# Kernel tuning notes

Measured on AMD Instinct MI355X. Metric: run time of the kernel, lower is better.

Reference implementation:

```python
import jax, jax.numpy as jnp
import numpy as np

TEMPERATURE = 0.0005

def conv1d(x, w, b):
    # x: [B,Cin,T], w: [Cout,Cin,K], 'same' padding as ConvNorm (pad=(K-1)//2)
    pad = (w.shape[-1] - 1) // 2
    y = jax.lax.conv_general_dilated(x, w, window_strides=(1,), padding=[(pad, pad)],
                                     dimension_numbers=('NCH', 'OIH', 'NCH'))
    return y + b[None, :, None]

def setup_inputs() -> dict:
    key = jax.random.key(0)
    ks = jax.random.split(key, 20)
    B, C_MEL, C_TXT, C_ATT, T1, T2 = 32, 80, 512, 80, 1600, 400
    s = 0.02
    return {
        'queries': jax.random.normal(ks[0], (B, C_MEL, T1), jnp.float32),
        'keys': jax.random.normal(ks[1], (B, C_TXT, T2), jnp.float32),
        'mask': jax.random.randint(ks[2], (B, T2, 1), 0, 2).astype(bool),
        'attn_prior': jax.random.uniform(ks[3], (B, T1, T2), jnp.float32),
        'speaker_embed': jax.random.normal(ks[4], (B, C_TXT), jnp.float32),
        # key_proj: Conv(512->1024,k3) -> ReLU -> Conv(1024->80,k1)
        'Wk1': jax.random.normal(ks[5], (C_TXT * 2, C_TXT, 3)) * s,
        'bk1': jax.random.normal(ks[6], (C_TXT * 2,)) * s,
        'Wk2': jax.random.normal(ks[7], (C_ATT, C_TXT * 2, 1)) * s,
        'bk2': jax.random.normal(ks[8], (C_ATT,)) * s,
        # query_proj: Conv(80->160,k3) -> ReLU -> Conv(160->80,k1) -> ReLU -> Conv(80->80,k1)
        'Wq1': jax.random.normal(ks[9], (C_MEL * 2, C_MEL, 3)) * s,
        'bq1': jax.random.normal(ks[10], (C_MEL * 2,)) * s,
        'Wq2': jax.random.normal(ks[11], (C_MEL, C_MEL * 2, 1)) * s,
        'bq2': jax.random.normal(ks[12], (C_MEL,)) * s,
        'Wq3': jax.random.normal(ks[13], (C_ATT, C_MEL, 1)) * s,
        'bq3': jax.random.normal(ks[14], (C_ATT,)) * s,
        # speaker projections (multi_speaker=True)
        'Wks': jax.random.normal(ks[15], (C_TXT, C_TXT)) * s,
        'bks': jax.random.normal(ks[16], (C_TXT,)) * s,
        'Wqs': jax.random.normal(ks[17], (C_MEL, C_TXT)) * s,
        'bqs': jax.random.normal(ks[18], (C_MEL,)) * s,
    }

def reference(queries, keys, mask, attn_prior, speaker_embed,
              Wk1, bk1, Wk2, bk2, Wq1, bq1, Wq2, bq2, Wq3, bq3,
              Wks, bks, Wqs, bqs):
    # speaker conditioning: Linear(spk) broadcast over time, added channelwise
    keys = keys + (speaker_embed @ Wks.T + bks)[:, :, None]
    queries = queries + (speaker_embed @ Wqs.T + bqs)[:, :, None]
    # projections
    k = jax.nn.relu(conv1d(keys, Wk1, bk1))
    k = conv1d(k, Wk2, bk2)                      # [B, C_att, T2]
    q = jax.nn.relu(conv1d(queries, Wq1, bq1))
    q = jax.nn.relu(conv1d(q, Wq2, bq2))
    q = conv1d(q, Wq3, bq3)                      # [B, C_att, T1]
    # -temp * sum_c (q-k)^2 == -temp * (||q||^2 + ||k||^2 - 2 q.k)
    q2 = jnp.sum(q * q, axis=1)                  # [B, T1]
    k2 = jnp.sum(k * k, axis=1)                  # [B, T2]
    qk = jnp.einsum('bct,bcs->bts', q, k)        # [B, T1, T2]
    attn = -TEMPERATURE * (q2[:, :, None] + k2[:, None, :] - 2.0 * qk)
    attn = attn[:, None]                         # [B, 1, T1, T2]
    attn = jax.nn.log_softmax(attn, axis=3) + jnp.log(attn_prior[:, None] + 1e-8)
    attn_logprob = attn
    m = jnp.transpose(mask, (0, 2, 1))[:, :, None, :]  # [B,1,1,T2]
    attn = jnp.where(m, -jnp.inf, attn)
    attn = jax.nn.softmax(attn, axis=3)
    return attn, attn_logprob
```

## Files before the change

kernel.cpp:

```cpp
#include <hip/hip_runtime.h>
#include <math.h>

#define TEMP 0.0005f
#define B_    32
#define CMEL  80
#define CTXT  512
#define T1_   1600
#define T2_   400

typedef short short8 __attribute__((ext_vector_type(8)));
typedef float f32x4 __attribute__((ext_vector_type(4)));

__device__ inline unsigned short f2bf(float f) {
    unsigned u = __float_as_uint(f);
    u += 0x7FFF + ((u >> 16) & 1);
    return (unsigned short)(u >> 16);
}
__device__ inline unsigned pack2(float a, float b) {
    return (unsigned)f2bf(a) | ((unsigned)f2bf(b) << 16);
}
__device__ inline float bf2f(unsigned short v) { return __uint_as_float(((unsigned)v) << 16); }

__global__ void prep_kernel(const float* __restrict__ se,
                            const float* __restrict__ Wks, const float* __restrict__ bks,
                            const float* __restrict__ Wqs, const float* __restrict__ bqs,
                            float* __restrict__ kb, float* __restrict__ qb,
                            const float* __restrict__ Wk1, const float* __restrict__ Wk2,
                            const float* __restrict__ Wq1, const float* __restrict__ Wq2,
                            const float* __restrict__ Wq3,
                            unsigned short* __restrict__ Ab1, unsigned short* __restrict__ A2,
                            unsigned short* __restrict__ A3, unsigned short* __restrict__ A4,
                            unsigned short* __restrict__ A5) {
    if (blockIdx.x < 74) {
        int tid = blockIdx.x * blockDim.x + threadIdx.x;
        const int nk = B_ * CTXT;
        if (tid < nk) {
            int b = tid / CTXT, c = tid % CTXT;
            const float4* s4 = reinterpret_cast<const float4*>(se + b * CTXT);
            const float4* w4 = reinterpret_cast<const float4*>(Wks + (size_t)c * CTXT);
            float acc = bks[c];
            #pragma unroll 4
            for (int j = 0; j < CTXT / 4; ++j) {
                float4 a = s4[j], w = w4[j];
                acc += a.x * w.x + a.y * w.y + a.z * w.z + a.w * w.w;
            }
            kb[tid] = acc;
        } else if (tid < nk + B_ * CMEL) {
            int t = tid - nk;
            int b = t / CMEL, c = t % CMEL;
            const float4* s4 = reinterpret_cast<const float4*>(se + b * CTXT);
            const float4* w4 = reinterpret_cast<const float4*>(Wqs + (size_t)c * CTXT);
            float acc = bqs[c];
            #pragma unroll 4
            for (int j = 0; j < CTXT / 4; ++j) {
                float4 a = s4[j], w = w4[j];
                acc += a.x * w.x + a.y * w.y + a.z * w.z + a.w * w.w;
            }
            qb[t] = acc;
        }
        return;
    }
    int e = (blockIdx.x - 74) * 256 + threadIdx.x;
    const int n1 = 1572864, n2 = 81920, n3 = 46080, n4 = 12800, n5 = 7680;
    if (e < n1) {
        int co = e / 1536, rem = e - co * 1536;
        int dt = rem >> 9, ci = rem & 511;
        Ab1[e] = f2bf(Wk1[((size_t)co * 512 + ci) * 3 + dt]);
    } else if ((e -= n1) < n2) {
        A2[e] = f2bf(Wk2[e]);
    } else if ((e -= n2) < n3) {
        int co = e / 288, rem = e - co * 288;
        int dt = rem / 96, cc = rem - dt * 96;
        A3[e] = (cc < 80) ? f2bf(Wq1[((size_t)co * 80 + cc) * 3 + dt]) : 0;
    } else if ((e -= n3) < n4) {
        A4[e] = f2bf(Wq2[e]);
    } else if ((e -= n4) < n5) {
        int co = e / 96, cc = e - co * 96;
        A5[e] = (cc < 80) ? f2bf(Wq3[co * 80 + cc]) : 0;
    }
}

__global__ void castXk_kernel(const float* __restrict__ keys, const float* __restrict__ kb,
                              unsigned short* __restrict__ Xt) {
    __shared__ float tile[64][65];
    const int b = blockIdx.z;
    const int row0 = blockIdx.x * 64;
    const int ci0 = blockIdx.y * 64;
    const int tid = threadIdx.x;
    #pragma unroll
    for (int i = 0; i < 16; ++i) {
        int linear = i * 256 + tid;
        int ci_l = linear >> 6, t_l = linear & 63;
        int t = row0 + t_l - 1;
        float v = 0.f;
        if (t >= 0 && t < 400)
            v = keys[((size_t)b * 512 + ci0 + ci_l) * 400 + t] + kb[b * 512 + ci0 + ci_l];
        tile[t_l][ci_l] = v;
    }
    __syncthreads();
    #pragma unroll
    for (int i = 0; i < 16; ++i) {
        int linear = i * 256 + tid;
        int t_l = linear >> 6, ci_l = linear & 63;
        int row = row0 + t_l;
        if (row < 456)
            Xt[((size_t)b * 456 + row) * 512 + ci0 + ci_l] = f2bf(tile[t_l][ci_l]);
    }
}

__global__ __launch_bounds__(256) void castXq_kernel(
        const float* __restrict__ q, const float* __restrict__ qb,
        unsigned short* __restrict__ Xq1) {
    __shared__ float tile[80][65];
    const int b = blockIdx.y;
    const int t0 = blockIdx.x * 64;
    const int tid = threadIdx.x;
    if (t0 == 0 && tid < 48)
        ((unsigned*)(Xq1 + (size_t)b * 1602 * 96))[tid] = 0u;
    if (t0 == 1536 && tid < 48)
        ((unsigned*)(Xq1 + ((size_t)b * 1602 + 1601) * 96))[tid] = 0u;
    {
        int tl = tid & 63, c0 = tid >> 6;
        for (int c = c0; c < 80; c += 4)
            tile[c][tl] = q[((size_t)b * 80 + c) * 1600 + t0 + tl] + qb[b * 80 + c];
    }
    __syncthreads();
    int row = tid >> 2, cg = tid & 3;
    int t = t0 + row;
    unsigned* orow = (unsigned*)(Xq1 + ((size_t)b * 1602 + t + 1) * 96 + cg * 24);
    #pragma unroll
    for (int jj = 0; jj < 12; ++jj) {
        int c0 = cg * 24 + jj * 2, c1 = c0 + 1;
        float f0 = (c0 < 80) ? tile[c0][row] : 0.f;
        float f1 = (c1 < 80) ? tile[c1][row] : 0.f;
        orow[jj] = pack2(f0, f1);
    }
}

__global__ __launch_bounds__(256) void conv1k_mfma(
        const unsigned short* __restrict__ Ab, const unsigned short* __restrict__ Xt,
        const float* __restrict__ bias, unsigned short* __restrict__ k1c) {
    __shared__ short As[3 * 128 * 40];
    __shared__ short Xs[66 * 40];
    const int b = blockIdx.z;
    const int co0 = blockIdx.y * 128;
    const int t0 = blockIdx.x * 64;
    const int tid = threadIdx.x;
    const int lane = tid & 63, w = tid >> 6;
    const int wm = w >> 1, wn = w & 1;
    const int l15 = lane & 15, quad = lane >> 4;
    f32x4 acc[4][2];
    #pragma unroll
    for (int mt = 0; mt < 4; ++mt)
        #pragma unroll
        for (int nt = 0; nt < 2; ++nt)
            acc[mt][nt] = (f32x4){0.f, 0.f, 0.f, 0.f};

    for (int ci0 = 0; ci0 < 512; ci0 += 32) {
        __syncthreads();
        #pragma unroll
        for (int i = 0; i < 6; ++i) {
            int linear = i * 256 + tid;
            int dt = linear >> 9;
            int rem = linear & 511;
            int r = rem >> 2, c16 = rem & 3;
            int4 v = *(const int4*)(Ab + (size_t)(co0 + r) * 1536 + dt * 512 + ci0 + c16 * 8);
            *(int4*)(As + (dt * 128 + r) * 40 + c16 * 8) = v;
        }
        #pragma unroll
        for (int i = 0; i < 2; ++i) {
            int c = i * 256 + tid;
            if (c < 264) {
                int row = c >> 2, c16 = c & 3;
                int4 v = *(const int4*)(Xt + ((size_t)b * 456 + t0 + row) * 512 + ci0 + c16 * 8);
                *(int4*)(Xs + row * 40 + c16 * 8) = v;
            }
        }
        __syncthreads();
        #pragma unroll
        for (int dt = 0; dt < 3; ++dt) {
            short8 af[4], bfr[2];
            #pragma unroll
            for (int mt = 0; mt < 4; ++mt)
                af[mt] = *(const short8*)(As + (dt * 128 + wm * 64 + mt * 16 + l15) * 40 + quad * 8);
            #pragma unroll
            for (int nt = 0; nt < 2; ++nt)
                bfr[nt] = *(const short8*)(Xs + (wn * 32 + nt * 16 + l15 + dt) * 40 + quad * 8);
            #pragma unroll
            for (int mt = 0; mt < 4; ++mt)
                #pragma unroll
                for (int nt = 0; nt < 2; ++nt)
                    acc[mt][nt] = __builtin_amdgcn_mfma_f32_16x16x32_bf16(af[mt], bfr[nt], acc[mt][nt], 0, 0, 0);
        }
    }
    #pragma unroll
    for (int mt = 0; mt < 4; ++mt) {
        int cob = co0 + wm * 64 + mt * 16 + quad * 4;
        float bv[4];
        #pragma unroll
        for (int r = 0; r < 4; ++r) bv[r] = bias[cob + r];
        #pragma unroll
        for (int nt = 0; nt < 2; ++nt) {
            int t = t0 + wn * 32 + nt * 16 + l15;
            if (t >= 400) continue;
            float v0 = fmaxf(acc[mt][nt][0] + bv[0], 0.f);
            float v1 = fmaxf(acc[mt][nt][1] + bv[1], 0.f);
            float v2 = fmaxf(acc[mt][nt][2] + bv[2], 0.f);
            float v3 = fmaxf(acc[mt][nt][3] + bv[3], 0.f);
            uint2 p;
            p.x = pack2(v0, v1);
            p.y = pack2(v2, v3);
            *(uint2*)(k1c + ((size_t)b * 400 + t) * 1024 + cob) = p;
        }
    }
}

template<int MT, int NKC, int DTC, bool RELU, int OMODE, int INW, int OUTW, int N, int NR>
__global__ __launch_bounds__(256) void gemm_cl(
        const unsigned short* __restrict__ A, const unsigned short* __restrict__ X,
        const float* __restrict__ bias, unsigned short* __restrict__ out) {
    const int b = blockIdx.y;
    const int tid = threadIdx.x;
    const int lane = tid & 63, w = tid >> 6;
    const int l15 = lane & 15, quad = lane >> 4;
    const int s = blockIdx.x * 64 + w * 16 + l15;
    const int srow = (s < N) ? s : (N - 1);
    const unsigned short* xb = X + (size_t)b * NR * INW;

    f32x4 acc[MT];
    #pragma unroll
    for (int mt = 0; mt < MT; ++mt) acc[mt] = (f32x4){0.f, 0.f, 0.f, 0.f};

    #pragma unroll
    for (int kc = 0; kc < NKC; ++kc) {
        const int dt = DTC ? (kc / DTC) : 0;
        const int koff = DTC ? ((kc - dt * DTC) * 32) : (kc * 32);
        short8 bfr = *(const short8*)(xb + (size_t)(srow + dt) * INW + koff + quad * 8);
        #pragma unroll
        for (int mt = 0; mt < MT; ++mt) {
            short8 af = *(const short8*)(A + (size_t)(mt * 16 + l15) * (NKC * 32) + kc * 32 + quad * 8);
            acc[mt] = __builtin_amdgcn_mfma_f32_16x16x32_bf16(af, bfr, acc[mt], 0, 0, 0);
        }
    }
    if (s >= N) return;

    float v[MT][4];
    float ss = 0.f;
    #pragma unroll
    for (int mt = 0; mt < MT; ++mt) {
        #pragma unroll
        for (int r = 0; r < 4; ++r) {
            float x = acc[mt][r] + bias[mt * 16 + quad * 4 + r];
            if (RELU) x = fmaxf(x, 0.f);
            v[mt][r] = x;
            if (OMODE >= 2) ss += x * x;
        }
    }
    if (OMODE >= 2) {
        ss += __shfl_xor(ss, 16, 64);
        ss += __shfl_xor(ss, 32, 64);
    }
    unsigned short* orow = out + ((size_t)b * N + s) * OUTW;
    #pragma unroll
    for (int mt = 0; mt < MT; ++mt) {
        uint2 p;
        p.x = pack2(v[mt][0], v[mt][1]);
        p.y = pack2(v[mt][2], v[mt][3]);
        *(uint2*)(orow + mt * 16 + quad * 4) = p;
    }
    if (OMODE == 1 && quad == 0) {
        uint4 z = {0u, 0u, 0u, 0u};
        *(uint4*)(orow + 80) = z;
        *(uint4*)(orow + 88) = z;
    }
    if (OMODE >= 2 && quad == 0) {
        float e80 = (OMODE == 2) ? (-0.5f * ss) : 1.0f;
        float e81 = (OMODE == 2) ? 1.0f : (-0.5f * ss);
        uint4 z0 = {pack2(e80, e81), 0u, 0u, 0u};
        uint4 z1 = {0u, 0u, 0u, 0u};
        *(uint4*)(orow + 80) = z0;
        *(uint4*)(orow + 88) = z1;
    }
}

__global__ __launch_bounds__(256) void gemm_k2_kernel(
        const unsigned short* __restrict__ A, const unsigned short* __restrict__ X,
        const float* __restrict__ bias, unsigned short* __restrict__ out) {
    __shared__ float red[3][64][21];
    const int b = blockIdx.y;
    const int tid = threadIdx.x, lane = tid & 63, w = tid >> 6;
    const int l15 = lane & 15, quad = lane >> 4;
    const int s = blockIdx.x * 16 + l15;
    const unsigned short* xb = X + ((size_t)b * 400 + s) * 1024 + quad * 8;
    f32x4 acc[5];
    #pragma unroll
    for (int mt = 0; mt < 5; ++mt) acc[mt] = (f32x4){0.f, 0.f, 0.f, 0.f};
    #pragma unroll
    for (int kk = 0; kk < 8; ++kk) {
        int kc = w * 8 + kk;
        short8 bfr = *(const short8*)(xb + kc * 32);
        #pragma unroll
        for (int mt = 0; mt < 5; ++mt) {
            short8 af = *(const short8*)(A + (size_t)(mt * 16 + l15) * 1024 + kc * 32 + quad * 8);
            acc[mt] = __builtin_amdgcn_mfma_f32_16x16x32_bf16(af, bfr, acc[mt], 0, 0, 0);
        }
    }
    if (w > 0) {
        #pragma unroll
        for (int mt = 0; mt < 5; ++mt)
            #pragma unroll
            for (int r = 0; r < 4; ++r)
                red[w - 1][lane][mt * 4 + r] = acc[mt][r];
    }
    __syncthreads();
    if (w != 0) return;
    #pragma unroll
    for (int wv = 0; wv < 3; ++wv)
        #pragma unroll
        for (int mt = 0; mt < 5; ++mt)
            #pragma unroll
            for (int r = 0; r < 4; ++r)
                acc[mt][r] += red[wv][lane][mt * 4 + r];
    float v[5][4];
    float ss = 0.f;
    #pragma unroll
    for (int mt = 0; mt < 5; ++mt)
        #pragma unroll
        for (int r = 0; r < 4; ++r) {
            float x = acc[mt][r] + bias[mt * 16 + quad * 4 + r];
            v[mt][r] = x;
            ss += x * x;
        }
    ss += __shfl_xor(ss, 16, 64);
    ss += __shfl_xor(ss, 32, 64);
    unsigned short* orow = out + ((size_t)b * 400 + s) * 96;
    #pragma unroll
    for (int mt = 0; mt < 5; ++mt) {
        uint2 p;
        p.x = pack2(v[mt][0], v[mt][1]);
        p.y = pack2(v[mt][2], v[mt][3]);
        *(uint2*)(orow + mt * 16 + quad * 4) = p;
    }
    if (quad == 0) {
        uint4 z0 = {pack2(-0.5f * ss, 1.0f), 0u, 0u, 0u};
        uint4 z1 = {0u, 0u, 0u, 0u};
        *(uint4*)(orow + 80) = z0;
        *(uint4*)(orow + 88) = z1;
    }
}

__global__ __launch_bounds__(64) void attn_logits_kernel(
        const unsigned short* __restrict__ qT, const unsigned short* __restrict__ kT,
        unsigned short* __restrict__ lgt) {
    const int b = blockIdx.y;
    const int t10 = blockIdx.x * 16;
    const int lane = threadIdx.x;
    const int l15 = lane & 15, quad = lane >> 4;

    const unsigned short* qrow = qT + ((size_t)b * T1_ + t10 + l15) * 96;
    short8 af[3];
    #pragma unroll
    for (int kc = 0; kc < 3; ++kc)
        af[kc] = *(const short8*)(qrow + kc * 32 + quad * 8);

    f32x4 acc[25];
    #pragma unroll
    for (int ns = 0; ns < 25; ++ns) acc[ns] = (f32x4){0.f, 0.f, 0.f, 0.f};
    const unsigned short* kbase = kT + (size_t)b * T2_ * 96 + l15 * 96 + quad * 8;
    #pragma unroll
    for (int ns = 0; ns < 25; ++ns) {
        #pragma unroll
        for (int kc = 0; kc < 3; ++kc) {
            short8 bf = *(const short8*)(kbase + ns * 16 * 96 + kc * 32);
            acc[ns] = __builtin_amdgcn_mfma_f32_16x16x32_bf16(af[kc], bf, acc[ns], 0, 0, 0);
        }
    }
    const float K2T = 2.0f * TEMP;
    #pragma unroll
    for (int r = 0; r < 4; ++r) {
        unsigned short* orow = lgt + ((size_t)b * T1_ + t10 + quad * 4 + r) * T2_;
        #pragma unroll
        for (int ns = 0; ns < 25; ++ns)
            orow[ns * 16 + l15] = f2bf(K2T * acc[ns][r]);
    }
}

__global__ __launch_bounds__(256) void softmax_kernel(
        const unsigned short* __restrict__ lgt, const int* __restrict__ mask,
        const float* __restrict__ prior,
        float* __restrict__ attn_out, float* __restrict__ lp_out) {
    const int b = blockIdx.y;
    const int t1 = blockIdx.x * 4 + (threadIdx.x >> 6);
    const int lane = threadIdx.x & 63;
    const unsigned short* lrow = lgt + ((size_t)b * T1_ + t1) * T2_;
    const float* prow = prior + ((size_t)b * T1_ + t1) * T2_;
    const int* mrow = mask + b * T2_;

    float l[7], pe[7], kp[7];
    #pragma unroll
    for (int j = 0; j < 7; ++j) {
        int s = lane + 64 * j;
        bool v = (j < 6) || (lane < 16);
        l[j]  = v ? bf2f(lrow[s]) : -1e30f;
        pe[j] = v ? (prow[s] + 1e-8f) : 1.f;
        kp[j] = (v && !mrow[v ? s : 0]) ? 1.f : 0.f;
    }
    float m = l[0];
    #pragma unroll
    for (int j = 1; j < 7; ++j) m = fmaxf(m, l[j]);
    #pragma unroll
    for (int off = 1; off <= 32; off <<= 1) m = fmaxf(m, __shfl_xor(m, off, 64));
    float e1[7];
    float sum = 0.f;
    #pragma unroll
    for (int j = 0; j < 7; ++j) { float e = __expf(l[j] - m); e1[j] = e; sum += e; }
    #pragma unroll
    for (int off = 1; off <= 32; off <<= 1) sum += __shfl_xor(sum, off, 64);
    const float lse = m + __logf(sum);

    float u[7];
    float sum2 = 0.f;
    #pragma unroll
    for (int j = 0; j < 7; ++j) {
        float uu = e1[j] * pe[j] * kp[j];
        u[j] = uu;
        sum2 += uu;
    }
    #pragma unroll
    for (int off = 1; off <= 32; off <<= 1) sum2 += __shfl_xor(sum2, off, 64);
    const float inv = 1.f / sum2;

    float* lpr = lp_out + ((size_t)b * T1_ + t1) * T2_;
    float* atr = attn_out + ((size_t)b * T1_ + t1) * T2_;
    #pragma unroll
    for (int j = 0; j < 7; ++j) {
        int s = lane + 64 * j;
        bool v = (j < 6) || (lane < 16);
        if (v) {
            lpr[s] = l[j] - lse + __logf(pe[j]);
            atr[s] = u[j] * inv;
        }
    }
}

extern "C" void kernel_launch(void* const* d_in, const int* in_sizes, int n_in,
                              void* d_out, int out_size, void* d_ws, size_t ws_size,
                              hipStream_t stream) {
    const float* queries = (const float*)d_in[0];
    const float* keys    = (const float*)d_in[1];
    const int*   mask    = (const int*)d_in[2];
    const float* prior   = (const float*)d_in[3];
    const float* se      = (const float*)d_in[4];
    const float* Wk1 = (const float*)d_in[5];
    const float* bk1 = (const float*)d_in[6];
    const float* Wk2 = (const float*)d_in[7];
    const float* bk2 = (const float*)d_in[8];
    const float* Wq1 = (const float*)d_in[9];
    const float* bq1 = (const float*)d_in[10];
    const float* Wq2 = (const float*)d_in[11];
    const float* bq2 = (const float*)d_in[12];
    const float* Wq3 = (const float*)d_in[13];
    const float* bq3 = (const float*)d_in[14];
    const float* Wks = (const float*)d_in[15];
    const float* bks = (const float*)d_in[16];
    const float* Wqs = (const float*)d_in[17];
    const float* bqs = (const float*)d_in[18];

    float* ws = (float*)d_ws;
    float* kb = ws;
    float* qb = ws + 16384;
    unsigned short* Ab1 = (unsigned short*)(ws + 18944);
    unsigned short* A2  = (unsigned short*)(ws + 805376);
    unsigned short* A3  = (unsigned short*)(ws + 846336);
    unsigned short* A4  = (unsigned short*)(ws + 869376);
    unsigned short* A5  = (unsigned short*)(ws + 875776);
    unsigned short* qT  = (unsigned short*)(ws + 879616);
    unsigned short* kT  = (unsigned short*)(ws + 3337216);
    const size_t D = 3951616;
    unsigned short* Xk  = (unsigned short*)(ws + D);
    unsigned short* k1c = (unsigned short*)(ws + D + 3735552);
    unsigned short* Xq1 = (unsigned short*)(ws + D);
    unsigned short* Xq2 = (unsigned short*)(ws + D + 2460672);
    unsigned short* Xq3 = (unsigned short*)(ws + D);
    unsigned short* lgt = (unsigned short*)(ws + D);

    float* attn_out = (float*)d_out;
    float* lp_out   = attn_out + (size_t)B_ * T1_ * T2_;

    prep_kernel<<<dim3(6798), dim3(256), 0, stream>>>(se, Wks, bks, Wqs, bqs, kb, qb,
                                                      Wk1, Wk2, Wq1, Wq2, Wq3,
                                                      Ab1, A2, A3, A4, A5);
    castXk_kernel<<<dim3(8, 8, 32), dim3(256), 0, stream>>>(keys, kb, Xk);
    conv1k_mfma<<<dim3(7, 8, 32), dim3(256), 0, stream>>>(Ab1, Xk, bk1, k1c);
    gemm_k2_kernel<<<dim3(25, 32), 256, 0, stream>>>(A2, k1c, bk2, kT);
    castXq_kernel<<<dim3(25, 32), dim3(256), 0, stream>>>(queries, qb, Xq1);
    gemm_cl<10, 9, 3, true, 0, 96, 160, 1600, 1602>
        <<<dim3(25, 32), 256, 0, stream>>>(A3, Xq1, bq1, Xq2);
    gemm_cl<5, 5, 0, true, 1, 160, 96, 1600, 1600>
        <<<dim3(25, 32), 256, 0, stream>>>(A4, Xq2, bq2, Xq3);
    gemm_cl<5, 3, 0, false, 3, 96, 96, 1600, 1600>
        <<<dim3(25, 32), 256, 0, stream>>>(A5, Xq3, bq3, qT);
    attn_logits_kernel<<<dim3(100, 32), dim3(64), 0, stream>>>(qT, kT, lgt);
    softmax_kernel<<<dim3(400, 32), dim3(256), 0, stream>>>(lgt, mask, prior, attn_out, lp_out);
}
```

Measured before the change: 514.1 us.

## Fuse three query projection GEMMs into one kernel via LDS intermediates

Replaces the three separate query-path GEMM launches with a single kernel. The kernel keeps each 64-row tile's intermediate activations in shared memory between the conv3, 1x1 and 1x1 layers. This removes two global writes and reads of the intermediate buffers and two kernel launches. It raises LDS use per block, which may lower occupancy.

```diff
diff --git a/kernel.cpp b/kernel.cpp
--- a/kernel.cpp
+++ b/kernel.cpp
@@ -215,74 +215,6 @@
     }
 }
 
-template<int MT, int NKC, int DTC, bool RELU, int OMODE, int INW, int OUTW, int N, int NR>
-__global__ __launch_bounds__(256) void gemm_cl(
-        const unsigned short* __restrict__ A, const unsigned short* __restrict__ X,
-        const float* __restrict__ bias, unsigned short* __restrict__ out) {
-    const int b = blockIdx.y;
-    const int tid = threadIdx.x;
-    const int lane = tid & 63, w = tid >> 6;
-    const int l15 = lane & 15, quad = lane >> 4;
-    const int s = blockIdx.x * 64 + w * 16 + l15;
-    const int srow = (s < N) ? s : (N - 1);
-    const unsigned short* xb = X + (size_t)b * NR * INW;
-
-    f32x4 acc[MT];
-    #pragma unroll
-    for (int mt = 0; mt < MT; ++mt) acc[mt] = (f32x4){0.f, 0.f, 0.f, 0.f};
-
-    #pragma unroll
-    for (int kc = 0; kc < NKC; ++kc) {
-        const int dt = DTC ? (kc / DTC) : 0;
-        const int koff = DTC ? ((kc - dt * DTC) * 32) : (kc * 32);
-        short8 bfr = *(const short8*)(xb + (size_t)(srow + dt) * INW + koff + quad * 8);
-        #pragma unroll
-        for (int mt = 0; mt < MT; ++mt) {
-            short8 af = *(const short8*)(A + (size_t)(mt * 16 + l15) * (NKC * 32) + kc * 32 + quad * 8);
-            acc[mt] = __builtin_amdgcn_mfma_f32_16x16x32_bf16(af, bfr, acc[mt], 0, 0, 0);
-        }
-    }
-    if (s >= N) return;
-
-    float v[MT][4];
-    float ss = 0.f;
-    #pragma unroll
-    for (int mt = 0; mt < MT; ++mt) {
-        #pragma unroll
-        for (int r = 0; r < 4; ++r) {
-            float x = acc[mt][r] + bias[mt * 16 + quad * 4 + r];
-            if (RELU) x = fmaxf(x, 0.f);
-            v[mt][r] = x;
-            if (OMODE >= 2) ss += x * x;
-        }
-    }
-    if (OMODE >= 2) {
-        ss += __shfl_xor(ss, 16, 64);
-        ss += __shfl_xor(ss, 32, 64);
-    }
-    unsigned short* orow = out + ((size_t)b * N + s) * OUTW;
-    #pragma unroll
-    for (int mt = 0; mt < MT; ++mt) {
-        uint2 p;
-        p.x = pack2(v[mt][0], v[mt][1]);
-        p.y = pack2(v[mt][2], v[mt][3]);
-        *(uint2*)(orow + mt * 16 + quad * 4) = p;
-    }
-    if (OMODE == 1 && quad == 0) {
-        uint4 z = {0u, 0u, 0u, 0u};
-        *(uint4*)(orow + 80) = z;
-        *(uint4*)(orow + 88) = z;
-    }
-    if (OMODE >= 2 && quad == 0) {
-        float e80 = (OMODE == 2) ? (-0.5f * ss) : 1.0f;
-        float e81 = (OMODE == 2) ? 1.0f : (-0.5f * ss);
-        uint4 z0 = {pack2(e80, e81), 0u, 0u, 0u};
-        uint4 z1 = {0u, 0u, 0u, 0u};
-        *(uint4*)(orow + 80) = z0;
-        *(uint4*)(orow + 88) = z1;
-    }
-}
-
 __global__ __launch_bounds__(256) void gemm_k2_kernel(
         const unsigned short* __restrict__ A, const unsigned short* __restrict__ X,
         const float* __restrict__ bias, unsigned short* __restrict__ out) {
@@ -346,6 +278,119 @@
         uint4 z1 = {0u, 0u, 0u, 0u};
         *(uint4*)(orow + 80) = z0;
         *(uint4*)(orow + 88) = z1;
+    }
+}
+
+__global__ __launch_bounds__(256) void qpath_fused(
+        const unsigned short* __restrict__ A3, const unsigned short* __restrict__ A4,
+        const unsigned short* __restrict__ A5, const unsigned short* __restrict__ Xq1,
+        const float* __restrict__ bq1, const float* __restrict__ bq2,
+        const float* __restrict__ bq3, unsigned short* __restrict__ qT) {
+    __shared__ short LA[64 * 168];
+    __shared__ short LB[64 * 104];
+    const int b = blockIdx.y;
+    const int t0 = blockIdx.x * 64;
+    const int tid = threadIdx.x;
+    const int lane = tid & 63, w = tid >> 6;
+    const int l15 = lane & 15, quad = lane >> 4;
+    const int row = w * 16 + l15;
+    const int s = t0 + row;
+    const unsigned short* xb = Xq1 + (size_t)b * 1602 * 96;
+
+    {
+        f32x4 acc[10];
+        #pragma unroll
+        for (int mt = 0; mt < 10; ++mt) acc[mt] = (f32x4){0.f, 0.f, 0.f, 0.f};
+        #pragma unroll
+        for (int kc = 0; kc < 9; ++kc) {
+            const int dt = kc / 3, koff = (kc - dt * 3) * 32;
+            short8 bfr = *(const short8*)(xb + (size_t)(s + dt) * 96 + koff + quad * 8);
+            #pragma unroll
+            for (int mt = 0; mt < 10; ++mt) {
+                short8 af = *(const short8*)(A3 + (size_t)(mt * 16 + l15) * 288 + kc * 32 + quad * 8);
+                acc[mt] = __builtin_amdgcn_mfma_f32_16x16x32_bf16(af, bfr, acc[mt], 0, 0, 0);
+            }
+        }
+        #pragma unroll
+        for (int mt = 0; mt < 10; ++mt) {
+            float x0 = fmaxf(acc[mt][0] + bq1[mt * 16 + quad * 4 + 0], 0.f);
+            float x1 = fmaxf(acc[mt][1] + bq1[mt * 16 + quad * 4 + 1], 0.f);
+            float x2 = fmaxf(acc[mt][2] + bq1[mt * 16 + quad * 4 + 2], 0.f);
+            float x3 = fmaxf(acc[mt][3] + bq1[mt * 16 + quad * 4 + 3], 0.f);
+            uint2 p;
+            p.x = pack2(x0, x1);
+            p.y = pack2(x2, x3);
+            *(uint2*)(LA + row * 168 + mt * 16 + quad * 4) = p;
+        }
+    }
+
+    {
+        f32x4 acc[5];
+        #pragma unroll
+        for (int mt = 0; mt < 5; ++mt) acc[mt] = (f32x4){0.f, 0.f, 0.f, 0.f};
+        #pragma unroll
+        for (int kc = 0; kc < 5; ++kc) {
+            short8 bfr = *(const short8*)(LA + row * 168 + kc * 32 + quad * 8);
+            #pragma unroll
+            for (int mt = 0; mt < 5; ++mt) {
+                short8 af = *(const short8*)(A4 + (size_t)(mt * 16 + l15) * 160 + kc * 32 + quad * 8);
+                acc[mt] = __builtin_amdgcn_mfma_f32_16x16x32_bf16(af, bfr, acc[mt], 0, 0, 0);
+            }
+        }
+        #pragma unroll
+        for (int mt = 0; mt < 5; ++mt) {
+            float x0 = fmaxf(acc[mt][0] + bq2[mt * 16 + quad * 4 + 0], 0.f);
+            float x1 = fmaxf(acc[mt][1] + bq2[mt * 16 + quad * 4 + 1], 0.f);
+            float x2 = fmaxf(acc[mt][2] + bq2[mt * 16 + quad * 4 + 2], 0.f);
+            float x3 = fmaxf(acc[mt][3] + bq2[mt * 16 + quad * 4 + 3], 0.f);
+            uint2 p;
+            p.x = pack2(x0, x1);
+            p.y = pack2(x2, x3);
+            *(uint2*)(LB + row * 104 + mt * 16 + quad * 4) = p;
+        }
+        uint2 z = {0u, 0u};
+        *(uint2*)(LB + row * 104 + 80 + quad * 4) = z;
+    }
+
+    {
+        f32x4 acc[5];
+        #pragma unroll
+        for (int mt = 0; mt < 5; ++mt) acc[mt] = (f32x4){0.f, 0.f, 0.f, 0.f};
+        #pragma unroll
+        for (int kc = 0; kc < 3; ++kc) {
+            short8 bfr = *(const short8*)(LB + row * 104 + kc * 32 + quad * 8);
+            #pragma unroll
+            for (int mt = 0; mt < 5; ++mt) {
+                short8 af = *(const short8*)(A5 + (size_t)(mt * 16 + l15) * 96 + kc * 32 + quad * 8);
+                acc[mt] = __builtin_amdgcn_mfma_f32_16x16x32_bf16(af, bfr, acc[mt], 0, 0, 0);
+            }
+        }
+        float v[5][4];
+        float ss = 0.f;
+        #pragma unroll
+        for (int mt = 0; mt < 5; ++mt)
+            #pragma unroll
+            for (int r = 0; r < 4; ++r) {
+                float x = acc[mt][r] + bq3[mt * 16 + quad * 4 + r];
+                v[mt][r] = x;
+                ss += x * x;
+            }
+        ss += __shfl_xor(ss, 16, 64);
+        ss += __shfl_xor(ss, 32, 64);
+        unsigned short* orow = qT + ((size_t)b * T1_ + s) * 96;
+        #pragma unroll
+        for (int mt = 0; mt < 5; ++mt) {
+            uint2 p;
+            p.x = pack2(v[mt][0], v[mt][1]);
+            p.y = pack2(v[mt][2], v[mt][3]);
+            *(uint2*)(orow + mt * 16 + quad * 4) = p;
+        }
+        if (quad == 0) {
+            uint4 z0 = {pack2(1.0f, -0.5f * ss), 0u, 0u, 0u};
+            uint4 z1 = {0u, 0u, 0u, 0u};
+            *(uint4*)(orow + 80) = z0;
+            *(uint4*)(orow + 88) = z1;
+        }
     }
 }
 
@@ -480,8 +525,6 @@
     unsigned short* Xk  = (unsigned short*)(ws + D);
     unsigned short* k1c = (unsigned short*)(ws + D + 3735552);
     unsigned short* Xq1 = (unsigned short*)(ws + D);
-    unsigned short* Xq2 = (unsigned short*)(ws + D + 2460672);
-    unsigned short* Xq3 = (unsigned short*)(ws + D);
     unsigned short* lgt = (unsigned short*)(ws + D);
 
     float* attn_out = (float*)d_out;
@@ -494,12 +537,8 @@
     conv1k_mfma<<<dim3(7, 8, 32), dim3(256), 0, stream>>>(Ab1, Xk, bk1, k1c);
     gemm_k2_kernel<<<dim3(25, 32), 256, 0, stream>>>(A2, k1c, bk2, kT);
     castXq_kernel<<<dim3(25, 32), dim3(256), 0, stream>>>(queries, qb, Xq1);
-    gemm_cl<10, 9, 3, true, 0, 96, 160, 1600, 1602>
-        <<<dim3(25, 32), 256, 0, stream>>>(A3, Xq1, bq1, Xq2);
-    gemm_cl<5, 5, 0, true, 1, 160, 96, 1600, 1600>
-        <<<dim3(25, 32), 256, 0, stream>>>(A4, Xq2, bq2, Xq3);
-    gemm_cl<5, 3, 0, false, 3, 96, 96, 1600, 1600>
-        <<<dim3(25, 32), 256, 0, stream>>>(A5, Xq3, bq3, qT);
+    qpath_fused<<<dim3(25, 32), dim3(256), 0, stream>>>(A3, A4, A5, Xq1,
+                                                        bq1, bq2, bq3, qT);
     attn_logits_kernel<<<dim3(100, 32), dim3(64), 0, stream>>>(qT, kT, lgt);
     softmax_kernel<<<dim3(400, 32), dim3(256), 0, stream>>>(lgt, mask, prior, attn_out, lp_out);
 }
```

Result: faster. 503.1 us (-2.1%).
